# Kernel optimization log

Measured on AMD Instinct MI355X. Metric: run time of the kernel, lower is better.

The kernel has to match this reference:

```python
import jax, jax.numpy as jnp
import numpy as np

B, C, L = 4, 512, 4096
H = 8
DH = C // H
MLP = 2048


def _ln(x, g, b, eps=1e-5):
    mu = x.mean(-1, keepdims=True)
    var = ((x - mu) ** 2).mean(-1, keepdims=True)
    return (x - mu) / jnp.sqrt(var + eps) * g + b


def setup_inputs() -> dict:
    key = jax.random.key(0)
    ks = jax.random.split(key, 16)
    s = 0.02
    d = {
        "x": jax.random.normal(ks[0], (B, C, L), jnp.float32),
        "Wq": jax.random.normal(ks[1], (C, C), jnp.float32) * s,
        "bq": jnp.zeros((C,), jnp.float32),
        "gq": jnp.ones((C,), jnp.float32),
        "betaq": jnp.zeros((C,), jnp.float32),
        "Wk": jax.random.normal(ks[2], (C, C), jnp.float32) * s,
        "bk": jnp.zeros((C,), jnp.float32),
        "gk": jnp.ones((C,), jnp.float32),
        "betak": jnp.zeros((C,), jnp.float32),
        "Wv": jax.random.normal(ks[3], (C, C), jnp.float32) * s,
        "bv": jnp.zeros((C,), jnp.float32),
        "gv": jnp.ones((C,), jnp.float32),
        "betav": jnp.zeros((C,), jnp.float32),
        "Wkq": jax.random.normal(ks[4], (C, C), jnp.float32) * s,
        "bkq": jnp.zeros((C,), jnp.float32),
        "Wkk": jax.random.normal(ks[5], (C, C), jnp.float32) * s,
        "bkk": jnp.zeros((C,), jnp.float32),
        "g_attn": jnp.ones((C,), jnp.float32),
        "b_attn": jnp.zeros((C,), jnp.float32),
        "W1": jax.random.normal(ks[6], (C, MLP), jnp.float32) * s,
        "b1": jnp.zeros((MLP,), jnp.float32),
        "W2": jax.random.normal(ks[7], (MLP, C), jnp.float32) * s,
        "b2": jnp.zeros((C,), jnp.float32),
    }
    return d


def _split_heads(t):
    # [B, L, C] -> [B, H, L, DH]
    b, l, _ = t.shape
    return t.reshape(b, l, H, DH).transpose(0, 2, 1, 3)


def reference(x, Wq, bq, gq, betaq, Wk, bk, gk, betak, Wv, bv, gv, betav,
              Wkq, bkq, Wkk, bkk, g_attn, b_attn, W1, b1, W2, b2):
    # x: [B, C, L] -> flatten(2).permute(0,2,1) -> [B, L, C]
    xf = jnp.transpose(x, (0, 2, 1))
    Q = _ln(xf @ Wq + bq, gq, betaq)            # [B, L, C]
    K = _ln(xf @ Wk + bk, gk, betak)            # [B, L, C]
    V = _ln(xf @ Wv + bv, gv, betav)            # [B, L, C]
    # add zero token to K, V (seq dim)
    z = jnp.zeros((x.shape[0], 1, C), x.dtype)
    K = jnp.concatenate([z, K], axis=1)         # [B, Lk, C], Lk = L+1
    V = jnp.concatenate([z, V], axis=1)
    phiQ = jnp.tanh(Q @ Wkq + bkq) + 1.0        # [B, L, C]
    phiK = jnp.tanh(K @ Wkk + bkk) + 1.0        # [B, Lk, C]

    Qh, Kh, Vh = _split_heads(Q), _split_heads(K), _split_heads(V)
    pQ, pK = _split_heads(phiQ), _split_heads(phiK)  # [B,H,L,DH], [B,H,Lk,DH]

    # softmax-reweighted phi_K: score from mean-query probe against K
    q_probe = Qh.mean(axis=2)                                   # [B,H,DH]
    score = jnp.einsum('bhd,bhld->bhl', q_probe, Kh) / jnp.sqrt(jnp.float32(DH))
    score = jax.nn.softmax(score, axis=-1)                      # [B,H,Lk]
    pKw = pK * score[..., None]                                 # [B,H,Lk,DH]

    kv = jnp.einsum('bhld,bhle->bhde', pKw, Vh)                 # [B,H,DH,DH]
    num = jnp.einsum('bhqd,bhde->bhqe', pQ, kv)                 # [B,H,L,DH]
    ksum = pKw.sum(axis=2)                                      # [B,H,DH]
    bottom = jnp.einsum('bhqd,bhd->bhq', pQ, ksum)[..., None] + 1e-6
    out_h = num / bottom                                        # [B,H,L,DH]

    out = out_h.transpose(0, 2, 1, 3).reshape(x.shape[0], -1, C)  # [B,L,C]
    a = _ln(out, g_attn, b_attn)
    m = jax.nn.gelu(a @ W1 + b1, approximate=False) @ W2 + b2
    res = a + m                                                 # residual MLP
    res = jnp.transpose(res, (0, 2, 1))                         # [B,C,L]
    return res + x
```

## Files before the change

kernel.cpp:

```cpp
#include <hip/hip_runtime.h>
#include <math.h>

#define B_ 4
#define C_ 512
#define L_ 4096
#define H_ 8
#define DH_ 64
#define MLP_ 2048
#define BL_ (B_*L_)
#define LK_ (L_+1)

typedef _Float16 f16;
typedef _Float16 f16x8 __attribute__((ext_vector_type(8)));
typedef _Float16 f16x4 __attribute__((ext_vector_type(4)));
typedef float f32x4 __attribute__((ext_vector_type(4)));

__device__ __forceinline__ void gl16(void* lds, const void* g) {
  __builtin_amdgcn_global_load_lds((const __attribute__((address_space(1))) void*)g,
                                   (__attribute__((address_space(3))) void*)lds,
                                   16, 0, 0);
}

__device__ __forceinline__ float frcp(float x) { return __builtin_amdgcn_rcpf(x); }

__global__ __launch_bounds__(256) void transpose_w5(const float* __restrict__ Wq,
                                                    const float* __restrict__ Wk,
                                                    const float* __restrict__ Wv,
                                                    const float* __restrict__ Wkq,
                                                    const float* __restrict__ Wkk,
                                                    f16* __restrict__ dst) {
  int z = blockIdx.z;
  const float* W = (z == 0) ? Wq : (z == 1) ? Wk : (z == 2) ? Wv : (z == 3) ? Wkq : Wkk;
  f16* Wt = dst + (size_t)z * C_ * C_;
  __shared__ float tile[32][33];
  int n0 = blockIdx.x * 32, k0 = blockIdx.y * 32;
  int tx = threadIdx.x & 31, ty = threadIdx.x >> 5;
#pragma unroll
  for (int i = 0; i < 4; ++i)
    tile[ty + i * 8][tx] = W[(size_t)(k0 + ty + i * 8) * C_ + n0 + tx];
  __syncthreads();
#pragma unroll
  for (int i = 0; i < 4; ++i)
    Wt[(size_t)(n0 + ty + i * 8) * C_ + k0 + tx] = (f16)tile[tx][ty + i * 8];
}

__global__ __launch_bounds__(256) void transpose_w(const float* __restrict__ W,
                                                   f16* __restrict__ Wt, int K, int N) {
  __shared__ float tile[32][33];
  int n0 = blockIdx.x * 32, k0 = blockIdx.y * 32;
  int tx = threadIdx.x & 31, ty = threadIdx.x >> 5;
#pragma unroll
  for (int i = 0; i < 4; ++i)
    tile[ty + i * 8][tx] = W[(size_t)(k0 + ty + i * 8) * N + n0 + tx];
  __syncthreads();
#pragma unroll
  for (int i = 0; i < 4; ++i)
    Wt[(size_t)(n0 + ty + i * 8) * K + k0 + tx] = (f16)tile[tx][ty + i * 8];
}

__global__ __launch_bounds__(256) void transpose_x(const float* __restrict__ x,
                                                   f16* __restrict__ xf) {
  __shared__ float tile[32][33];
  int b = blockIdx.z;
  int l0 = blockIdx.x * 32, c0 = blockIdx.y * 32;
  int tx = threadIdx.x & 31, ty = threadIdx.x >> 5;
#pragma unroll
  for (int i = 0; i < 4; ++i)
    tile[ty + i * 8][tx] = x[((size_t)b * C_ + c0 + ty + i * 8) * L_ + l0 + tx];
  __syncthreads();
#pragma unroll
  for (int i = 0; i < 4; ++i)
    xf[((size_t)b * L_ + l0 + ty + i * 8) * C_ + c0 + tx] = (f16)tile[tx][ty + i * 8];
}

__global__ __launch_bounds__(256) void pack_params(
    const float* bq, const float* bk, const float* bv,
    const float* gq, const float* gk, const float* gv,
    const float* betaq, const float* betak, const float* betav,
    const float* bkq, const float* bkk,
    float* bqkv, float* gqkv, float* betaqkv, float* bphi) {
  int i = blockIdx.x * 256 + threadIdx.x;
  int w = i >> 9, c = i & 511;
  bqkv[i]    = (w == 0 ? bq : (w == 1 ? bk : bv))[c];
  gqkv[i]    = (w == 0 ? gq : (w == 1 ? gk : gv))[c];
  betaqkv[i] = (w == 0 ? betaq : (w == 1 ? betak : betav))[c];
  if (i < 1024) bphi[i] = (i < 512) ? bkq[i] : bkk[i - 512];
}

template <int EPI>
__global__ __launch_bounds__(256, 2) void gemm64(const f16* __restrict__ A,
                                                 const f16* __restrict__ Bt,
                                                 const float* __restrict__ bias,
                                                 f16* __restrict__ Ch,
                                                 int N, int K,
                                                 const float* __restrict__ Bot,
                                                 const f16* __restrict__ Ares,
                                                 const float* __restrict__ Xres,
                                                 float* __restrict__ Fout,
                                                 long long zA, long long zB,
                                                 long long zC, long long zBias,
                                                 long long zBot) {
  __shared__ f16 smem[2 * 128 * 128];
  A  += (size_t)blockIdx.z * zA;
  Bt += (size_t)blockIdx.z * zB;
  if (EPI != 6) Ch += (size_t)blockIdx.z * zC;
  if (EPI == 3) Bot += (size_t)blockIdx.z * zBot;
  else          bias += (size_t)blockIdx.z * zBias;

  const int tid = threadIdx.x;
  const int lane = tid & 63, wv = tid >> 6;
  const int wm = wv >> 1, wn = wv & 1;
  const int bm = blockIdx.x * 128, bn = blockIdx.y * 128;
  const int l15 = lane & 15, q = lane >> 4;

  const int srow = tid >> 3;
  const int schunk = (tid & 7) ^ (srow & 7);
  const f16* pa = A + (size_t)(bm + srow) * K + schunk * 8;
  const f16* pb = Bt + (size_t)(bn + srow) * K + schunk * 8;
  f16* la = smem + tid * 8;
  f16* lb = smem + 8192 + tid * 8;
  const int sw0 = (q ^ (lane & 7)) * 8;
  const int sw1 = ((4 + q) ^ (lane & 7)) * 8;

  f32x4 acc[4][4] = {};

#pragma unroll
  for (int p = 0; p < 4; ++p) gl16(la + p * 2048, pa + (size_t)p * 32 * K);
#pragma unroll
  for (int p = 0; p < 4; ++p) gl16(lb + p * 2048, pb + (size_t)p * 32 * K);

  int cur = 0;
  for (int k0 = 0; k0 < K; k0 += 64) {
    __syncthreads();
    const int nxt = cur ^ 1;
    if (k0 + 64 < K) {
#pragma unroll
      for (int p = 0; p < 4; ++p) gl16(la + nxt * 16384 + p * 2048, pa + (size_t)p * 32 * K + k0 + 64);
#pragma unroll
      for (int p = 0; p < 4; ++p) gl16(lb + nxt * 16384 + p * 2048, pb + (size_t)p * 32 * K + k0 + 64);
    }
    const f16* As = smem + cur * 16384;
    const f16* Bs = As + 8192;
#pragma unroll
    for (int ks = 0; ks < 2; ++ks) {
      const int sw = ks ? sw1 : sw0;
      f16x8 af[4], bf[4];
#pragma unroll
      for (int i = 0; i < 4; ++i)
        af[i] = *(const f16x8*)&As[(wm * 64 + i * 16 + l15) * 64 + sw];
#pragma unroll
      for (int j = 0; j < 4; ++j)
        bf[j] = *(const f16x8*)&Bs[(wn * 64 + j * 16 + l15) * 64 + sw];
#pragma unroll
      for (int i = 0; i < 4; ++i)
#pragma unroll
        for (int j = 0; j < 4; ++j)
          acc[i][j] = __builtin_amdgcn_mfma_f32_16x16x32_f16(af[i], bf[j], acc[i][j], 0, 0, 0);
    }
    cur = nxt;
  }

  __syncthreads();
#pragma unroll
  for (int j = 0; j < 4; ++j) {
    int lc = wn * 64 + j * 16 + l15;
    float bb = (EPI == 3) ? 0.f : bias[bn + lc];
#pragma unroll
    for (int i = 0; i < 4; ++i) {
#pragma unroll
      for (int r = 0; r < 4; ++r) {
        int lr = wm * 64 + i * 16 + q * 4 + r;
        float v = acc[i][j][r] + bb;
        if (EPI == 1) {
          v = 2.0f * frcp(1.0f + __expf(-2.0f * v));
        } else if (EPI == 2) {
          v = v * frcp(1.0f + __expf(-1.5957691f * (v + 0.044715f * v * v * v)));
        } else if (EPI == 3) {
          v = v * frcp(Bot[(size_t)(bm + lr) * H_ + ((bn + lc) >> 6)] + 1e-6f);
        }
        smem[lr * 128 + ((((lc >> 3) ^ (lr & 15)) << 3) | (lc & 7))] = (f16)v;
      }
    }
  }
  __syncthreads();

  if (EPI != 6) {
#pragma unroll
    for (int p = 0; p < 8; ++p) {
      int idx = p * 256 + tid;
      int row = idx >> 4, ch = idx & 15;
      f16x8 vv = *(const f16x8*)&smem[row * 128 + ((ch ^ (row & 15)) << 3)];
      *(f16x8*)&Ch[(size_t)(bm + row) * N + bn + ch * 8] = vv;
    }
  } else {
#pragma unroll
    for (int p = 0; p < 8; ++p) {
      int idx = p * 256 + tid;
      int row = idx >> 4, ch = idx & 15;
      f16x8 av = *(const f16x8*)&Ares[(size_t)(bm + row) * C_ + bn + ch * 8];
      f16* sp = &smem[row * 128 + ((ch ^ (row & 15)) << 3)];
      f16x8 sv = *(const f16x8*)sp;
#pragma unroll
      for (int jj = 0; jj < 8; ++jj) sv[jj] = (f16)((float)sv[jj] + (float)av[jj]);
      *(f16x8*)sp = sv;
    }
    __syncthreads();
    int c = tid & 127, lh = tid >> 7;
    int b = bm >> 12, lbase = (bm & 4095) + lh * 64;
    const float* xp = Xres + ((size_t)b * C_ + bn + c) * L_ + lbase;
    float* op = Fout + ((size_t)b * C_ + bn + c) * L_ + lbase;
    int chi = c >> 3, clo = c & 7;
#pragma unroll
    for (int s = 0; s < 16; ++s) {
      int l = lh * 64 + s * 4;
      float4 xv = *(const float4*)(xp + s * 4);
      float4 r;
      r.x = (float)smem[(l + 0) * 128 + (((chi ^ ((l + 0) & 15)) << 3) | clo)] + xv.x;
      r.y = (float)smem[(l + 1) * 128 + (((chi ^ ((l + 1) & 15)) << 3) | clo)] + xv.y;
      r.z = (float)smem[(l + 2) * 128 + (((chi ^ ((l + 2) & 15)) << 3) | clo)] + xv.z;
      r.w = (float)smem[(l + 3) * 128 + (((chi ^ ((l + 3) & 15)) << 3) | clo)] + xv.w;
      *(float4*)(op + s * 4) = r;
    }
  }
}

__global__ __launch_bounds__(256) void ln16(const f16* __restrict__ X,
                                            const float* __restrict__ g,
                                            const float* __restrict__ bta,
                                            f16* __restrict__ Y, int threeway) {
  int wv = threadIdx.x >> 6, lane = threadIdx.x & 63;
  int r = blockIdx.x * 4 + wv;
  int token = r, which = 0;
  if (threeway) { token = r / 3; which = r - token * 3; }
  const f16* xr = X + (size_t)r * C_;
  f16x8 v = *(const f16x8*)(xr + lane * 8);
  float vals[8];
  float s = 0.f, s2 = 0.f;
#pragma unroll
  for (int j = 0; j < 8; ++j) { vals[j] = (float)v[j]; s += vals[j]; s2 += vals[j] * vals[j]; }
#pragma unroll
  for (int m_ = 1; m_ < 64; m_ <<= 1) { s += __shfl_xor(s, m_); s2 += __shfl_xor(s2, m_); }
  float mu = s * (1.f / C_);
  float var = s2 * (1.f / C_) - mu * mu;
  float rstd = rsqrtf(var + 1e-5f);
  const float* gp = g + which * C_;
  const float* bp = bta + which * C_;
  f16x8 o;
#pragma unroll
  for (int j = 0; j < 8; ++j) {
    int c = lane * 8 + j;
    o[j] = (f16)((vals[j] - mu) * rstd * gp[c] + bp[c]);
  }
  *(f16x8*)(Y + ((size_t)which * BL_ + token) * C_ + lane * 8) = o;
}

__global__ __launch_bounds__(256) void qprobe2(const f16* __restrict__ Q,
                                               float* __restrict__ qp) {
  int blk = blockIdx.x;
  int b = blk >> 6;
  int r0 = blk * 64;
  int t = threadIdx.x;
  int c8 = (t & 63) * 8, rg = t >> 6;
  float s[8] = {0.f, 0.f, 0.f, 0.f, 0.f, 0.f, 0.f, 0.f};
#pragma unroll
  for (int i = 0; i < 16; ++i) {
    const f16* row = Q + ((size_t)r0 + rg + i * 4) * C_ + c8;
    f16x8 v = *(const f16x8*)row;
#pragma unroll
    for (int j = 0; j < 8; ++j) s[j] += (float)v[j];
  }
  __shared__ float red[4][520];
#pragma unroll
  for (int j = 0; j < 8; ++j) red[rg][c8 + j] = s[j];
  __syncthreads();
  int c = t * 2;
  float a0 = red[0][c] + red[1][c] + red[2][c] + red[3][c];
  float a1 = red[0][c + 1] + red[1][c + 1] + red[2][c + 1] + red[3][c + 1];
  atomicAdd(&qp[b * C_ + c], a0);
  atomicAdd(&qp[b * C_ + c + 1], a1);
}

__global__ __launch_bounds__(256) void logits_kernel(const f16* __restrict__ Kh,
                                                     const float* __restrict__ qp,
                                                     float* __restrict__ score) {
  int wv = threadIdx.x >> 6, lane = threadIdx.x & 63;
  int token = blockIdx.x * 4 + wv;
  int b = token >> 12;
  int l = token & (L_ - 1);
  const f16* row = Kh + (size_t)token * C_;
  int h = lane >> 3, j0 = (lane & 7) * 8;
  const float* qph = qp + b * C_ + h * DH_ + j0;
  float p = 0.f;
#pragma unroll
  for (int j = 0; j < 8; ++j) p += qph[j] * (float)row[h * DH_ + j0 + j];
  p += __shfl_xor(p, 1); p += __shfl_xor(p, 2); p += __shfl_xor(p, 4);
  if ((lane & 7) == 0)
    score[((size_t)b * H_ + h) * LK_ + 1 + l] = p * (1.f / L_) * 0.125f;
}

__global__ __launch_bounds__(256) void softmax_kernel(float* __restrict__ score) {
  int bh = blockIdx.x, t = threadIdx.x;
  float* s = score + (size_t)bh * LK_;
  __shared__ float red[256];
  float mx = 0.f;
  for (int i = t; i < L_; i += 256) mx = fmaxf(mx, s[1 + i]);
  red[t] = mx; __syncthreads();
  for (int k = 128; k; k >>= 1) { if (t < k) red[t] = fmaxf(red[t], red[t + k]); __syncthreads(); }
  mx = red[0]; __syncthreads();
  float sum = (t == 0) ? expf(-mx) : 0.f;
  for (int i = t; i < L_; i += 256) { float e = expf(s[1 + i] - mx); s[1 + i] = e; sum += e; }
  red[t] = sum; __syncthreads();
  for (int k = 128; k; k >>= 1) { if (t < k) red[t] += red[t + k]; __syncthreads(); }
  float inv = 1.f / red[0];
  __syncthreads();
  for (int i = t; i < L_; i += 256) s[1 + i] *= inv;
  if (t == 0) s[0] = expf(-mx) * inv;
}

__global__ __launch_bounds__(256) void ksum_init(const float* __restrict__ score,
                                                 const float* __restrict__ bkk,
                                                 float* __restrict__ ksum) {
  int i = blockIdx.x * 256 + threadIdx.x;
  int bh = i >> 6, d = i & 63, h = bh & 7;
  float pk0 = tanhf(bkk[h * DH_ + d]) + 1.f;
  ksum[i] = score[(size_t)bh * LK_] * pk0;
}

#define PIDX(l, c) ((l) * 68 + (c))
#define AIDX(d, e) ((d) * 68 + (e) + ((((d) >> 3)) << 2))
__global__ __launch_bounds__(256, 2) void kv_part_kernel(const f16* __restrict__ phiK,
                                                         const f16* __restrict__ Vh,
                                                         const float* __restrict__ score,
                                                         float* __restrict__ kvp,
                                                         float* __restrict__ ksum) {
  __shared__ float sm0[4416];
  __shared__ float sm1[4416];
  int bh = blockIdx.y, b = bh >> 3, h = bh & 7;
  int part = blockIdx.x;
  int l0 = part * 256;
  int t = threadIdx.x, lane = t & 63, wv = t >> 6;
  int R = (lane >> 3) * 8, Cc = (lane & 7) * 8;
  float acc[8][8] = {};
  float ks[8] = {0.f, 0.f, 0.f, 0.f, 0.f, 0.f, 0.f, 0.f};

  for (int c = 0; c < 4; ++c) {
    int lc = l0 + c * 64;
    __syncthreads();
#pragma unroll
    for (int p = 0; p < 4; ++p) {
      int l = p * 16 + (t >> 4);
      int c4 = (t & 15) * 4;
      size_t grow = ((size_t)b * L_ + lc + l) * C_ + h * DH_ + c4;
      float w = score[(size_t)bh * LK_ + 1 + lc + l];
      f16x4 pk = *(const f16x4*)(phiK + grow);
      f16x4 vvv = *(const f16x4*)(Vh + grow);
      sm0[PIDX(l, c4) + 0] = w * (float)pk[0];
      sm0[PIDX(l, c4) + 1] = w * (float)pk[1];
      sm0[PIDX(l, c4) + 2] = w * (float)pk[2];
      sm0[PIDX(l, c4) + 3] = w * (float)pk[3];
      sm1[PIDX(l, c4) + 0] = (float)vvv[0];
      sm1[PIDX(l, c4) + 1] = (float)vvv[1];
      sm1[PIDX(l, c4) + 2] = (float)vvv[2];
      sm1[PIDX(l, c4) + 3] = (float)vvv[3];
    }
    __syncthreads();
#pragma unroll
    for (int i = 0; i < 16; ++i) {
      int ll = wv * 16 + i;
      float4 a0 = *(const float4*)&sm0[PIDX(ll, R)];
      float4 a1 = *(const float4*)&sm0[PIDX(ll, R + 4)];
      float4 b0 = *(const float4*)&sm1[PIDX(ll, Cc)];
      float4 b1 = *(const float4*)&sm1[PIDX(ll, Cc + 4)];
      float av[8] = {a0.x, a0.y, a0.z, a0.w, a1.x, a1.y, a1.z, a1.w};
      float bv2[8] = {b0.x, b0.y, b0.z, b0.w, b1.x, b1.y, b1.z, b1.w};
#pragma unroll
      for (int ii = 0; ii < 8; ++ii)
#pragma unroll
        for (int jj = 0; jj < 8; ++jj) acc[ii][jj] += av[ii] * bv2[jj];
      if ((lane & 7) == 0) {
#pragma unroll
        for (int ii = 0; ii < 8; ++ii) ks[ii] += av[ii];
      }
    }
  }

  __syncthreads();
  if ((lane & 7) == 0) {
#pragma unroll
    for (int i = 0; i < 8; ++i) sm1[wv * 64 + R + i] = ks[i];
  }
  for (int w = 0; w < 4; ++w) {
    if (wv == w) {
#pragma unroll
      for (int i = 0; i < 8; ++i) {
        float* p0 = &sm0[AIDX(R + i, Cc)];
        if (w == 0) {
          *(float4*)p0 = make_float4(acc[i][0], acc[i][1], acc[i][2], acc[i][3]);
          *(float4*)(p0 + 4) = make_float4(acc[i][4], acc[i][5], acc[i][6], acc[i][7]);
        } else {
          float4 o0 = *(const float4*)p0, o1 = *(const float4*)(p0 + 4);
          o0.x += acc[i][0]; o0.y += acc[i][1]; o0.z += acc[i][2]; o0.w += acc[i][3];
          o1.x += acc[i][4]; o1.y += acc[i][5]; o1.z += acc[i][6]; o1.w += acc[i][7];
          *(float4*)p0 = o0;
          *(float4*)(p0 + 4) = o1;
        }
      }
    }
    __syncthreads();
  }
  if (t < 64) {
    float s = sm1[t] + sm1[64 + t] + sm1[128 + t] + sm1[192 + t];
    atomicAdd(&ksum[bh * 64 + t], s);
  }
  float* dst = kvp + ((size_t)bh * 16 + part) * 4096;
#pragma unroll
  for (int i = 0; i < 16; ++i) {
    int idx = i * 256 + t;
    dst[idx] = sm0[AIDX(idx & 63, idx >> 6)];
  }
}

__global__ __launch_bounds__(256) void build_bd(const float* __restrict__ kvp,
                                                f16* __restrict__ BD) {
  size_t i = (size_t)blockIdx.x * 256 + threadIdx.x;
  int b = (int)(i >> 18);
  int nk = (int)(i & 262143);
  int n = nk >> 9, k = nk & 511;
  int hn = n >> 6, hk = k >> 6;
  float v = 0.f;
  if (hn == hk) {
    const float* p = kvp + ((size_t)(b * H_ + hn) * 16) * 4096 + (n & 63) * 64 + (k & 63);
#pragma unroll
    for (int pp = 0; pp < 16; ++pp) v += p[pp * 4096];
  }
  BD[i] = (f16)v;
}

__global__ __launch_bounds__(256) void bottom_kernel(const f16* __restrict__ phiQ,
                                                     const float* __restrict__ ksum,
                                                     float* __restrict__ bot) {
  int wv = threadIdx.x >> 6, lane = threadIdx.x & 63;
  int token = blockIdx.x * 4 + wv;
  int b = token >> 12;
  const f16* row = phiQ + (size_t)token * C_;
  int h = lane >> 3, j0 = (lane & 7) * 8;
  const float* ks = ksum + (b * H_ + h) * 64 + j0;
  float p = 0.f;
#pragma unroll
  for (int j = 0; j < 8; ++j) p += ks[j] * (float)row[h * DH_ + j0 + j];
  p += __shfl_xor(p, 1); p += __shfl_xor(p, 2); p += __shfl_xor(p, 4);
  if ((lane & 7) == 0) bot[(size_t)token * H_ + h] = p;
}

extern "C" void kernel_launch(void* const* d_in, const int* in_sizes, int n_in,
                              void* d_out, int out_size, void* d_ws, size_t ws_size,
                              hipStream_t stream) {
  (void)in_sizes; (void)n_in; (void)out_size; (void)ws_size;
  const float* x     = (const float*)d_in[0];
  const float* Wq    = (const float*)d_in[1];
  const float* bq    = (const float*)d_in[2];
  const float* gq    = (const float*)d_in[3];
  const float* betaq = (const float*)d_in[4];
  const float* Wk    = (const float*)d_in[5];
  const float* bk    = (const float*)d_in[6];
  const float* gk    = (const float*)d_in[7];
  const float* betak = (const float*)d_in[8];
  const float* Wv    = (const float*)d_in[9];
  const float* bv    = (const float*)d_in[10];
  const float* gv    = (const float*)d_in[11];
  const float* betav = (const float*)d_in[12];
  const float* Wkq   = (const float*)d_in[13];
  const float* bkq   = (const float*)d_in[14];
  const float* Wkk   = (const float*)d_in[15];
  const float* bkk   = (const float*)d_in[16];
  const float* g_at  = (const float*)d_in[17];
  const float* b_at  = (const float*)d_in[18];
  const float* W1    = (const float*)d_in[19];
  const float* b1    = (const float*)d_in[20];
  const float* W2    = (const float*)d_in[21];
  const float* b2    = (const float*)d_in[22];
  float* out = (float*)d_out;

  char* ws = (char*)d_ws;
  size_t off = 0;
  auto alloc = [&](size_t bytes) -> void* {
    void* p = ws + off;
    off += (bytes + 255) & ~(size_t)255;
    return p;
  };
  f16* U1    = (f16*)alloc((size_t)BL_ * MLP_ * 2);
  f16* QKVh  = (f16*)alloc((size_t)3 * BL_ * C_ * 2);
  f16* phiQK = (f16*)alloc((size_t)2 * BL_ * C_ * 2);
  f16* xf    = (f16*)alloc((size_t)BL_ * C_ * 2);
  f16* WqkvT = (f16*)alloc((size_t)3 * C_ * C_ * 2);
  f16* WkqT  = (f16*)alloc((size_t)C_ * C_ * 2);
  f16* WkkT  = (f16*)alloc((size_t)C_ * C_ * 2);
  f16* W1T   = (f16*)alloc((size_t)C_ * MLP_ * 2);
  f16* W2T   = (f16*)alloc((size_t)MLP_ * C_ * 2);
  f16* BD    = (f16*)alloc((size_t)B_ * C_ * C_ * 2);
  float* score = (float*)alloc((size_t)B_ * H_ * LK_ * 4);
  float* qp    = (float*)alloc((size_t)B_ * C_ * 4);
  float* kvp   = (float*)alloc((size_t)B_ * H_ * 16 * 4096 * 4);
  float* ksum  = (float*)alloc((size_t)B_ * H_ * DH_ * 4);
  float* bot   = (float*)alloc((size_t)BL_ * H_ * 4);
  float* bqkv    = (float*)alloc(1536 * 4);
  float* gqkv    = (float*)alloc(1536 * 4);
  float* betaqkv = (float*)alloc(1536 * 4);
  float* bphi    = (float*)alloc(1024 * 4);

  f16* tmpqkv = U1;
  f16* tmpA   = U1;
  f16* h1     = U1;
  f16* Qh = QKVh;
  f16* Kh = QKVh + (size_t)BL_ * C_;
  f16* Vh = QKVh + (size_t)2 * BL_ * C_;
  f16* ah = QKVh;
  f16* phiQ = phiQK;
  f16* phiK = phiQK + (size_t)BL_ * C_;

  dim3 blk(256);

  pack_params<<<6, blk, 0, stream>>>(bq, bk, bv, gq, gk, gv, betaq, betak, betav,
                                     bkq, bkk, bqkv, gqkv, betaqkv, bphi);

  transpose_w5<<<dim3(16, 16, 5), blk, 0, stream>>>(Wq, Wk, Wv, Wkq, Wkk, WqkvT);
  transpose_w<<<dim3(MLP_ / 32, C_ / 32), blk, 0, stream>>>(W1, W1T, C_, MLP_);
  transpose_w<<<dim3(C_ / 32, MLP_ / 32), blk, 0, stream>>>(W2, W2T, MLP_, C_);

  transpose_x<<<dim3(L_ / 32, C_ / 32, B_), blk, 0, stream>>>(x, xf);

  gemm64<5><<<dim3(BL_ / 128, 1536 / 128), blk, 0, stream>>>(
      xf, WqkvT, bqkv, tmpqkv, 1536, C_, nullptr, nullptr, nullptr, nullptr, 0, 0, 0, 0, 0);
  ln16<<<3 * BL_ / 4, blk, 0, stream>>>(tmpqkv, gqkv, betaqkv, QKVh, 1);

  hipMemsetAsync(qp, 0, (size_t)B_ * C_ * 4, stream);
  qprobe2<<<BL_ / 64, blk, 0, stream>>>(Qh, qp);

  gemm64<1><<<dim3(BL_ / 128, C_ / 128, 2), blk, 0, stream>>>(
      Qh, WkqT, bphi, phiQ, C_, C_, nullptr, nullptr, nullptr, nullptr,
      (long long)BL_ * C_, (long long)C_ * C_, (long long)BL_ * C_, (long long)C_, 0);

  logits_kernel<<<BL_ / 4, blk, 0, stream>>>(Kh, qp, score);
  softmax_kernel<<<B_ * H_, blk, 0, stream>>>(score);

  ksum_init<<<(B_ * H_ * DH_) / 256, blk, 0, stream>>>(score, bkk, ksum);
  kv_part_kernel<<<dim3(16, B_ * H_), blk, 0, stream>>>(phiK, Vh, score, kvp, ksum);

  build_bd<<<(B_ * C_ * C_) / 256, blk, 0, stream>>>(kvp, BD);
  bottom_kernel<<<BL_ / 4, blk, 0, stream>>>(phiQ, ksum, bot);

  gemm64<3><<<dim3(L_ / 128, C_ / 128, B_), blk, 0, stream>>>(
      phiQ, BD, nullptr, tmpA, C_, C_, bot, nullptr, nullptr, nullptr,
      (long long)L_ * C_, (long long)C_ * C_, (long long)L_ * C_, 0, (long long)L_ * H_);

  ln16<<<BL_ / 4, blk, 0, stream>>>(tmpA, g_at, b_at, ah, 0);

  gemm64<2><<<dim3(BL_ / 128, MLP_ / 128), blk, 0, stream>>>(
      ah, W1T, b1, h1, MLP_, C_, nullptr, nullptr, nullptr, nullptr, 0, 0, 0, 0, 0);
  gemm64<6><<<dim3(BL_ / 128, C_ / 128), blk, 0, stream>>>(
      h1, W2T, b2, nullptr, C_, MLP_, nullptr, ah, x, out, 0, 0, 0, 0, 0);
}
```

Before: 408.4 us.

## Use 32x32x16 MFMA in GEMM and merge small attention kernels

The shared GEMM template switches from 16x16x32 MFMA tiles (4x4 accumulators per wave) to 32x32x16 MFMA tiles (2x2 accumulators), which need fewer LDS fragment loads per MFMA. The epilogue row mapping is rewritten to match the 32x32 output layout. Separately, ksum_init is folded into the softmax kernel, and build_bd plus bottom_kernel are merged into one launch, cutting two kernel launches. The new LDS read pattern may cause different bank conflicts under the existing swizzle.

```diff
diff --git a/kernel.cpp b/kernel.cpp
--- a/kernel.cpp
+++ b/kernel.cpp
@@ -13,7 +13,7 @@
 typedef _Float16 f16;
 typedef _Float16 f16x8 __attribute__((ext_vector_type(8)));
 typedef _Float16 f16x4 __attribute__((ext_vector_type(4)));
-typedef float f32x4 __attribute__((ext_vector_type(4)));
+typedef float f32x16 __attribute__((ext_vector_type(16)));
 
 __device__ __forceinline__ void gl16(void* lds, const void* g) {
   __builtin_amdgcn_global_load_lds((const __attribute__((address_space(1))) void*)g,
@@ -111,7 +111,7 @@
   const int lane = tid & 63, wv = tid >> 6;
   const int wm = wv >> 1, wn = wv & 1;
   const int bm = blockIdx.x * 128, bn = blockIdx.y * 128;
-  const int l15 = lane & 15, q = lane >> 4;
+  const int r32 = lane & 31, kh = lane >> 5;
 
   const int srow = tid >> 3;
   const int schunk = (tid & 7) ^ (srow & 7);
@@ -119,10 +119,8 @@
   const f16* pb = Bt + (size_t)(bn + srow) * K + schunk * 8;
   f16* la = smem + tid * 8;
   f16* lb = smem + 8192 + tid * 8;
-  const int sw0 = (q ^ (lane & 7)) * 8;
-  const int sw1 = ((4 + q) ^ (lane & 7)) * 8;
-
-  f32x4 acc[4][4] = {};
+
+  f32x16 acc[2][2] = {};
 
 #pragma unroll
   for (int p = 0; p < 4; ++p) gl16(la + p * 2048, pa + (size_t)p * 32 * K);
@@ -142,35 +140,33 @@
     const f16* As = smem + cur * 16384;
     const f16* Bs = As + 8192;
 #pragma unroll
-    for (int ks = 0; ks < 2; ++ks) {
-      const int sw = ks ? sw1 : sw0;
-      f16x8 af[4], bf[4];
-#pragma unroll
-      for (int i = 0; i < 4; ++i)
-        af[i] = *(const f16x8*)&As[(wm * 64 + i * 16 + l15) * 64 + sw];
-#pragma unroll
-      for (int j = 0; j < 4; ++j)
-        bf[j] = *(const f16x8*)&Bs[(wn * 64 + j * 16 + l15) * 64 + sw];
-#pragma unroll
-      for (int i = 0; i < 4; ++i)
-#pragma unroll
-        for (int j = 0; j < 4; ++j)
-          acc[i][j] = __builtin_amdgcn_mfma_f32_16x16x32_f16(af[i], bf[j], acc[i][j], 0, 0, 0);
+    for (int s = 0; s < 4; ++s) {
+      const int sw = ((2 * s + kh) ^ (r32 & 7)) * 8;
+      f16x8 af[2], bf[2];
+      af[0] = *(const f16x8*)&As[(wm * 64 + r32) * 64 + sw];
+      af[1] = *(const f16x8*)&As[(wm * 64 + 32 + r32) * 64 + sw];
+      bf[0] = *(const f16x8*)&Bs[(wn * 64 + r32) * 64 + sw];
+      bf[1] = *(const f16x8*)&Bs[(wn * 64 + 32 + r32) * 64 + sw];
+#pragma unroll
+      for (int ti = 0; ti < 2; ++ti)
+#pragma unroll
+        for (int tj = 0; tj < 2; ++tj)
+          acc[ti][tj] = __builtin_amdgcn_mfma_f32_32x32x16_f16(af[ti], bf[tj], acc[ti][tj], 0, 0, 0);
     }
     cur = nxt;
   }
 
   __syncthreads();
 #pragma unroll
-  for (int j = 0; j < 4; ++j) {
-    int lc = wn * 64 + j * 16 + l15;
+  for (int tj = 0; tj < 2; ++tj) {
+    int lc = wn * 64 + tj * 32 + r32;
     float bb = (EPI == 3) ? 0.f : bias[bn + lc];
 #pragma unroll
-    for (int i = 0; i < 4; ++i) {
-#pragma unroll
-      for (int r = 0; r < 4; ++r) {
-        int lr = wm * 64 + i * 16 + q * 4 + r;
-        float v = acc[i][j][r] + bb;
+    for (int ti = 0; ti < 2; ++ti) {
+#pragma unroll
+      for (int reg = 0; reg < 16; ++reg) {
+        int lr = wm * 64 + ti * 32 + (reg & 3) + 8 * (reg >> 2) + 4 * kh;
+        float v = acc[ti][tj][reg] + bb;
         if (EPI == 1) {
           v = 2.0f * frcp(1.0f + __expf(-2.0f * v));
         } else if (EPI == 2) {
@@ -298,7 +294,9 @@
     score[((size_t)b * H_ + h) * LK_ + 1 + l] = p * (1.f / L_) * 0.125f;
 }
 
-__global__ __launch_bounds__(256) void softmax_kernel(float* __restrict__ score) {
+__global__ __launch_bounds__(256) void softmax_kernel(float* __restrict__ score,
+                                                      const float* __restrict__ bkk,
+                                                      float* __restrict__ ksum) {
   int bh = blockIdx.x, t = threadIdx.x;
   float* s = score + (size_t)bh * LK_;
   __shared__ float red[256];
@@ -314,16 +312,12 @@
   float inv = 1.f / red[0];
   __syncthreads();
   for (int i = t; i < L_; i += 256) s[1 + i] *= inv;
-  if (t == 0) s[0] = expf(-mx) * inv;
-}
-
-__global__ __launch_bounds__(256) void ksum_init(const float* __restrict__ score,
-                                                 const float* __restrict__ bkk,
-                                                 float* __restrict__ ksum) {
-  int i = blockIdx.x * 256 + threadIdx.x;
-  int bh = i >> 6, d = i & 63, h = bh & 7;
-  float pk0 = tanhf(bkk[h * DH_ + d]) + 1.f;
-  ksum[i] = score[(size_t)bh * LK_] * pk0;
+  float s0 = expf(-mx) * inv;
+  if (t == 0) s[0] = s0;
+  if (t < 64) {
+    int h = bh & 7;
+    ksum[bh * 64 + t] = s0 * (tanhf(bkk[h * DH_ + t]) + 1.f);
+  }
 }
 
 #define PIDX(l, c) ((l) * 68 + (c))
@@ -420,36 +414,37 @@
   }
 }
 
-__global__ __launch_bounds__(256) void build_bd(const float* __restrict__ kvp,
-                                                f16* __restrict__ BD) {
-  size_t i = (size_t)blockIdx.x * 256 + threadIdx.x;
-  int b = (int)(i >> 18);
-  int nk = (int)(i & 262143);
-  int n = nk >> 9, k = nk & 511;
-  int hn = n >> 6, hk = k >> 6;
-  float v = 0.f;
-  if (hn == hk) {
-    const float* p = kvp + ((size_t)(b * H_ + hn) * 16) * 4096 + (n & 63) * 64 + (k & 63);
-#pragma unroll
-    for (int pp = 0; pp < 16; ++pp) v += p[pp * 4096];
-  }
-  BD[i] = (f16)v;
-}
-
-__global__ __launch_bounds__(256) void bottom_kernel(const f16* __restrict__ phiQ,
-                                                     const float* __restrict__ ksum,
-                                                     float* __restrict__ bot) {
-  int wv = threadIdx.x >> 6, lane = threadIdx.x & 63;
-  int token = blockIdx.x * 4 + wv;
-  int b = token >> 12;
-  const f16* row = phiQ + (size_t)token * C_;
-  int h = lane >> 3, j0 = (lane & 7) * 8;
-  const float* ks = ksum + (b * H_ + h) * 64 + j0;
-  float p = 0.f;
-#pragma unroll
-  for (int j = 0; j < 8; ++j) p += ks[j] * (float)row[h * DH_ + j0 + j];
-  p += __shfl_xor(p, 1); p += __shfl_xor(p, 2); p += __shfl_xor(p, 4);
-  if ((lane & 7) == 0) bot[(size_t)token * H_ + h] = p;
+__global__ __launch_bounds__(256) void bd_bottom(const float* __restrict__ kvp,
+                                                 f16* __restrict__ BD,
+                                                 const f16* __restrict__ phiQ,
+                                                 const float* __restrict__ ksum,
+                                                 float* __restrict__ bot) {
+  if (blockIdx.x < 4096) {
+    size_t i = (size_t)blockIdx.x * 256 + threadIdx.x;
+    int b = (int)(i >> 18);
+    int nk = (int)(i & 262143);
+    int n = nk >> 9, k = nk & 511;
+    int hn = n >> 6, hk = k >> 6;
+    float v = 0.f;
+    if (hn == hk) {
+      const float* p = kvp + ((size_t)(b * H_ + hn) * 16) * 4096 + (n & 63) * 64 + (k & 63);
+#pragma unroll
+      for (int pp = 0; pp < 16; ++pp) v += p[pp * 4096];
+    }
+    BD[i] = (f16)v;
+  } else {
+    int wv = threadIdx.x >> 6, lane = threadIdx.x & 63;
+    int token = (blockIdx.x - 4096) * 4 + wv;
+    int b = token >> 12;
+    const f16* row = phiQ + (size_t)token * C_;
+    int h = lane >> 3, j0 = (lane & 7) * 8;
+    const float* ks = ksum + (b * H_ + h) * 64 + j0;
+    float p = 0.f;
+#pragma unroll
+    for (int j = 0; j < 8; ++j) p += ks[j] * (float)row[h * DH_ + j0 + j];
+    p += __shfl_xor(p, 1); p += __shfl_xor(p, 2); p += __shfl_xor(p, 4);
+    if ((lane & 7) == 0) bot[(size_t)token * H_ + h] = p;
+  }
 }
 
 extern "C" void kernel_launch(void* const* d_in, const int* in_sizes, int n_in,
@@ -526,7 +521,6 @@
   transpose_w5<<<dim3(16, 16, 5), blk, 0, stream>>>(Wq, Wk, Wv, Wkq, Wkk, WqkvT);
   transpose_w<<<dim3(MLP_ / 32, C_ / 32), blk, 0, stream>>>(W1, W1T, C_, MLP_);
   transpose_w<<<dim3(C_ / 32, MLP_ / 32), blk, 0, stream>>>(W2, W2T, MLP_, C_);
-
   transpose_x<<<dim3(L_ / 32, C_ / 32, B_), blk, 0, stream>>>(x, xf);
 
   gemm64<5><<<dim3(BL_ / 128, 1536 / 128), blk, 0, stream>>>(
@@ -541,13 +535,10 @@
       (long long)BL_ * C_, (long long)C_ * C_, (long long)BL_ * C_, (long long)C_, 0);
 
   logits_kernel<<<BL_ / 4, blk, 0, stream>>>(Kh, qp, score);
-  softmax_kernel<<<B_ * H_, blk, 0, stream>>>(score);
-
-  ksum_init<<<(B_ * H_ * DH_) / 256, blk, 0, stream>>>(score, bkk, ksum);
+  softmax_kernel<<<B_ * H_, blk, 0, stream>>>(score, bkk, ksum);
+
   kv_part_kernel<<<dim3(16, B_ * H_), blk, 0, stream>>>(phiK, Vh, score, kvp, ksum);
-
-  build_bd<<<(B_ * C_ * C_) / 256, blk, 0, stream>>>(kvp, BD);
-  bottom_kernel<<<BL_ / 4, blk, 0, stream>>>(phiQ, ksum, bot);
+  bd_bottom<<<8192, blk, 0, stream>>>(kvp, BD, phiQ, ksum, bot);
 
   gemm64<3><<<dim3(L_ / 128, C_ / 128, B_), blk, 0, stream>>>(
       phiQ, BD, nullptr, tmpA, C_, C_, bot, nullptr, nullptr, nullptr,
```

Result: slower. 429.3 us (+5.1%).
